# Performance work log

Measured on AMD Instinct MI355X. Metric: run time of the kernel, lower is better.

## Reference

```python
import jax, jax.numpy as jnp
import numpy as np

COUNT = 8  # hardcoded 8x8 patch grid in the original module


def setup_inputs() -> dict:
    key = jax.random.key(0)
    kx, = jax.random.split(key, 1)
    x = jax.random.normal(kx, (8, 64, 512, 512), dtype=jnp.float32)
    gamma = jnp.zeros((1,), dtype=jnp.float32)  # nn.Parameter(torch.zeros(1))
    return {"x": x, "gamma": gamma}


def reference(x, gamma):
    B, C, H, W = x.shape
    s = H // COUNT  # stride; original uses height-derived stride for both dims
    # Extract the 8x8 grid of patches without loops:
    # (B,C,H,W) -> (B,C,cnt,s,cnt,s) -> (B,cnt,cnt,C,s,s) -> (B,P,C,s*s)
    p = x.reshape(B, C, COUNT, s, COUNT, s)
    p = p.transpose(0, 2, 4, 1, 3, 5).reshape(B, COUNT * COUNT, C, s * s)
    # channel-channel energy per patch: [B,P,C,C]
    energy = jnp.einsum('bpci,bpdi->bpcd', p, p)
    # DANet trick: max - energy, then softmax over last dim
    energy_new = jnp.max(energy, axis=-1, keepdims=True) - energy
    attention = jax.nn.softmax(energy_new, axis=-1)
    out = jnp.einsum('bpcd,bpdi->bpci', attention, p)
    # reassemble spatial map
    out = out.reshape(B, COUNT, COUNT, C, s, s)
    out = out.transpose(0, 3, 1, 4, 2, 5).reshape(B, C, H, W)
    # NOTE: in the torch code y = x is an alias and x is overwritten in-place,
    # so the final result is gamma * attended + attended.
    return gamma[0] * out + out
```

## Files before the change

### kernel.cpp

```cpp
#include <hip/hip_runtime.h>


#define NW   512
#define HWs  262144
#define NS   16

typedef __attribute__((ext_vector_type(8)))  __bf16 bf8;
typedef __attribute__((ext_vector_type(4)))  __bf16 bf4;
typedef __attribute__((ext_vector_type(16))) float  f32x16;

#define F4E(v,j) ((j)==0?(v).x:(j)==1?(v).y:(j)==2?(v).z:(v).w)

__device__ __forceinline__ void bar_lgkm() {
  asm volatile("s_waitcnt lgkmcnt(0)" ::: "memory");
  __builtin_amdgcn_s_barrier();
}

extern "C" __global__ __launch_bounds__(512, 4)
void spectralAgg_kernel(const float* __restrict__ x, const float* __restrict__ g,
                        float* __restrict__ out) {
  __shared__ char lds[65536];
  char* sH = lds;
  char* sL = lds + 32768;
  char* sA = lds + 49152;

  const int T   = threadIdx.x;
  const int wv8 = T >> 6;
  const int l   = T & 63;
  const int l31 = l & 31;
  const int hh  = l >> 5;
  const int g2  = (T >> 4) & 3;
  const int e16 = T & 15;

  const int wg = blockIdx.x;
  const int b  = wg >> 6;
  const int pp = wg & 63;
  const size_t pbase = (size_t)b*64*HWs + (size_t)((pp>>3)*64)*NW + (size_t)((pp&7)*64);
  const float* xp = x + pbase;
  float* op = out + pbase;

  float4 ra[8];
#pragma unroll
  for (int k = 0; k < 8; ++k)
    ra[k] = *(const float4*)(xp + (size_t)(k*8+wv8)*HWs + (size_t)g2*NW + e16*4);

  const int q  = wv8 & 3;
  const int kh = wv8 >> 2;
  const int ct = q >> 1, dt = q & 1;
  const char* pA  = sH + (size_t)(ct*32+l31)*512 + kh*256;
  const char* pBh = sH + (size_t)(dt*32+l31)*512 + kh*256;
  const char* pBl = sL + (size_t)(dt*32+l31)*512 + kh*256;
  const int swz1 = (l31 & 15) << 4;

  f32x16 accG, accS;
#pragma unroll
  for (int r = 0; r < 16; ++r) { accG[r] = 0.f; accS[r] = 0.f; }

  for (int st = 0; st < NS; ++st) {
#pragma unroll
    for (int k = 0; k < 8; ++k) {
      const int c = k*8 + wv8;
      const float4 v = ra[k];
      bf4 h, lo;
      h[0]=(__bf16)v.x; h[1]=(__bf16)v.y; h[2]=(__bf16)v.z; h[3]=(__bf16)v.w;
      lo[0]=(__bf16)(v.x-(float)h[0]); lo[1]=(__bf16)(v.y-(float)h[1]);
      lo[2]=(__bf16)(v.z-(float)h[2]); lo[3]=(__bf16)(v.w-(float)h[3]);
      const int off = c*512 + ((g2*128 + e16*8) ^ ((c&15)<<4));
      *(bf4*)(sH+off) = h;
      *(bf4*)(sL+off) = lo;
    }
    const int sn = (st+1 < NS) ? st+1 : st;
#pragma unroll
    for (int k = 0; k < 8; ++k)
      ra[k] = *(const float4*)(xp + (size_t)(k*8+wv8)*HWs + (size_t)(sn*4+g2)*NW + e16*4);
    bar_lgkm();
#pragma unroll
    for (int k0 = 0; k0 < 8; ++k0) {
      const int off = (k0*32 + hh*16) ^ swz1;
      const bf8 a  = *(const bf8*)(pA  + off);
      const bf8 bh = *(const bf8*)(pBh + off);
      const bf8 bl = *(const bf8*)(pBl + off);
      accG = __builtin_amdgcn_mfma_f32_32x32x16_bf16(a, bh, accG, 0, 0, 0);
      accS = __builtin_amdgcn_mfma_f32_32x32x16_bf16(a, bl, accS, 0, 0, 0);
    }
    bar_lgkm();
  }

  float* E_lds = (float*)sH;
  float* S_lds = (float*)sL;
  if (kh == 0) {
#pragma unroll
    for (int r = 0; r < 16; ++r) {
      const int cr = ct*32 + (r&3) + ((r>>2)<<3) + (hh<<2);
      const int d  = dt*32 + l31;
      S_lds[cr*64+d] = accS[r];
      E_lds[cr*64+d] = accG[r] + accS[r];
    }
  }
  bar_lgkm();
  if (kh == 1) {
#pragma unroll
    for (int r = 0; r < 16; ++r) {
      const int cr = ct*32 + (r&3) + ((r>>2)<<3) + (hh<<2);
      const int d  = dt*32 + l31;
      S_lds[cr*64+d] += accS[r];
      E_lds[cr*64+d] += accG[r] + accS[r];
    }
  }
  bar_lgkm();
#pragma unroll
  for (int r = 0; r < 8; ++r) {
    const int c = T >> 3, d = (T&7)*8 + r;
    E_lds[c*64+d] += S_lds[d*64+c];
  }
  bar_lgkm();

  const int quad = (wv8*4+g2) & 15;
  const int rwb  = (wv8*4+g2) >> 4;
#pragma unroll
  for (int k = 0; k < 8; ++k) {
    const int cc = k & 3, mm = k >> 2;
    ra[k] = *(const float4*)(xp + (size_t)(quad*4+cc)*HWs + (size_t)(rwb+mm*2)*NW + e16*4);
  }

  const float gs = 1.0f + g[0];
#pragma unroll 1
  for (int rr = 0; rr < 8; ++rr) {
    const int c = wv8*8 + rr;
    const float e = E_lds[c*64 + l];
    float mn = e;
#pragma unroll
    for (int o = 32; o; o >>= 1) mn = fminf(mn, __shfl_xor(mn, o));
    const float w = __expf(mn - e);
    float s = w;
#pragma unroll
    for (int o = 32; o; o >>= 1) s += __shfl_xor(s, o);
    const float a = gs * w / s;
    *(__bf16*)(sA + c*256 + ((l*2) ^ ((c&15)<<4))) = (__bf16)a;
  }
  bar_lgkm();

  char* sT = sH;
  const char* pP = sT + (size_t)(wv8*32 + l31)*144;

  for (int st = 0; st < NS; ++st) {
#pragma unroll
    for (int mm = 0; mm < 2; ++mm) {
      const int row = rwb + mm*2;
#pragma unroll
      for (int jj = 0; jj < 4; ++jj) {
        const int i = row*64 + e16*4 + jj;
        bf4 qv;
        qv[0] = (__bf16)F4E(ra[mm*4+0], jj);
        qv[1] = (__bf16)F4E(ra[mm*4+1], jj);
        qv[2] = (__bf16)F4E(ra[mm*4+2], jj);
        qv[3] = (__bf16)F4E(ra[mm*4+3], jj);
        *(bf4*)(sT + i*144 + quad*8) = qv;
      }
    }
    const int sn = (st+1 < NS) ? st+1 : st;
#pragma unroll
    for (int k = 0; k < 8; ++k) {
      const int cc = k & 3, mm = k >> 2;
      ra[k] = *(const float4*)(xp + (size_t)(quad*4+cc)*HWs + (size_t)(sn*4+rwb+mm*2)*NW + e16*4);
    }
    bar_lgkm();

    f32x16 oo0, oo1;
#pragma unroll
    for (int r = 0; r < 16; ++r) { oo0[r] = 0.f; oo1[r] = 0.f; }
#pragma unroll
    for (int k0 = 0; k0 < 4; ++k0) {
      const int sAoff = (k0*32 + hh*16) ^ ((l31&15)<<4);
      const bf8 pa = *(const bf8*)(pP + k0*32 + hh*16);
      const bf8 b0 = *(const bf8*)(sA + (size_t)l31*256 + sAoff);
      const bf8 b1 = *(const bf8*)(sA + (size_t)(32+l31)*256 + sAoff);
      oo0 = __builtin_amdgcn_mfma_f32_32x32x16_bf16(pa, b0, oo0, 0, 0, 0);
      oo1 = __builtin_amdgcn_mfma_f32_32x32x16_bf16(pa, b1, oo1, 0, 0, 0);
    }

#pragma unroll
    for (int rq = 0; rq < 4; ++rq) {
      const int iloc = wv8*32 + rq*8 + hh*4;
      const int gi = st*256 + iloc;
      const int grow = gi >> 6, gcol = gi & 63;
      float* oprow = op + (size_t)grow*NW + gcol;
      float4 q0; q0.x = oo0[rq*4+0]; q0.y = oo0[rq*4+1];
                 q0.z = oo0[rq*4+2]; q0.w = oo0[rq*4+3];
      *(float4*)(oprow + (size_t)l31*HWs) = q0;
      float4 q1; q1.x = oo1[rq*4+0]; q1.y = oo1[rq*4+1];
                 q1.z = oo1[rq*4+2]; q1.w = oo1[rq*4+3];
      *(float4*)(oprow + (size_t)(32+l31)*HWs) = q1;
    }
    bar_lgkm();
  }
}

extern "C" void kernel_launch(void* const* d_in, const int* in_sizes, int n_in,
                              void* d_out, int out_size, void* d_ws, size_t ws_size,
                              hipStream_t stream) {
  const float* x = (const float*)d_in[0];
  const float* g = (const float*)d_in[1];
  float* o = (float*)d_out;
  spectralAgg_kernel<<<dim3(512), dim3(512), 0, stream>>>(x, g, o);
}
```

Before: 387.9 us.

## Double-buffer global loads, swizzle transpose LDS, hoist attention fragments, remap blocks

Both phases now keep two register sets of prefetched input tiles, so each global load is issued two stages ahead of use instead of one. The phase-3 transposed patch buffer moves from a padded 144-byte stride to a 256-byte XOR-swizzled layout, intended to avoid LDS bank conflicts. The attention B-fragments are loaded into registers once instead of per stage. Blocks are remapped so consecutive workgroups share a patch column across batch and row, which may change DRAM/L2 locality. Holding two prefetch sets raises register pressure, which could hurt occupancy under the 4-blocks launch bound.

New measurement: 447.5 us. +15.4%, slower.

```diff
diff --git a/kernel.cpp b/kernel.cpp
--- a/kernel.cpp
+++ b/kernel.cpp
@@ -14,6 +14,70 @@
 __device__ __forceinline__ void bar_lgkm() {
   asm volatile("s_waitcnt lgkmcnt(0)" ::: "memory");
   __builtin_amdgcn_s_barrier();
+}
+
+__device__ __forceinline__ void load1(const float* xp, int wv8, int g2, int e16,
+                                      int st, float4 (&R)[8]) {
+#pragma unroll
+  for (int k = 0; k < 8; ++k)
+    R[k] = *(const float4*)(xp + (size_t)(k*8+wv8)*HWs + (size_t)(st*4+g2)*NW + e16*4);
+}
+
+__device__ __forceinline__ void cvt1(char* sH, char* sL, int wv8, int g2, int e16,
+                                     const float4 (&R)[8]) {
+#pragma unroll
+  for (int k = 0; k < 8; ++k) {
+    const int c = k*8 + wv8;
+    const float4 v = R[k];
+    bf4 h, lo;
+    h[0]=(__bf16)v.x; h[1]=(__bf16)v.y; h[2]=(__bf16)v.z; h[3]=(__bf16)v.w;
+    lo[0]=(__bf16)(v.x-(float)h[0]); lo[1]=(__bf16)(v.y-(float)h[1]);
+    lo[2]=(__bf16)(v.z-(float)h[2]); lo[3]=(__bf16)(v.w-(float)h[3]);
+    const int off = c*512 + ((g2*128 + e16*8) ^ ((c&15)<<4));
+    *(bf4*)(sH+off) = h;
+    *(bf4*)(sL+off) = lo;
+  }
+}
+
+__device__ __forceinline__ void mfma1(const char* pA, const char* pBh, const char* pBl,
+                                      int hh, int swz1, f32x16& accG, f32x16& accS) {
+#pragma unroll
+  for (int k0 = 0; k0 < 8; ++k0) {
+    const int off = (k0*32 + hh*16) ^ swz1;
+    const bf8 a  = *(const bf8*)(pA  + off);
+    const bf8 bh = *(const bf8*)(pBh + off);
+    const bf8 bl = *(const bf8*)(pBl + off);
+    accG = __builtin_amdgcn_mfma_f32_32x32x16_bf16(a, bh, accG, 0, 0, 0);
+    accS = __builtin_amdgcn_mfma_f32_32x32x16_bf16(a, bl, accS, 0, 0, 0);
+  }
+}
+
+__device__ __forceinline__ void load3(const float* xp, int quad, int rwb, int e16,
+                                      int st, float4 (&R)[8]) {
+#pragma unroll
+  for (int k = 0; k < 8; ++k) {
+    const int cc = k & 3, mm = k >> 2;
+    R[k] = *(const float4*)(xp + (size_t)(quad*4+cc)*HWs + (size_t)(st*4+rwb+mm*2)*NW + e16*4);
+  }
+}
+
+__device__ __forceinline__ void cvt3(char* sT, int quad, int rwb, int e16,
+                                     const float4 (&R)[8]) {
+#pragma unroll
+  for (int mm = 0; mm < 2; ++mm) {
+    const int row = rwb + mm*2;
+#pragma unroll
+    for (int jj = 0; jj < 4; ++jj) {
+      const int i = row*64 + e16*4 + jj;
+      bf4 qv;
+      qv[0] = (__bf16)F4E(R[mm*4+0], jj);
+      qv[1] = (__bf16)F4E(R[mm*4+1], jj);
+      qv[2] = (__bf16)F4E(R[mm*4+2], jj);
+      qv[3] = (__bf16)F4E(R[mm*4+3], jj);
+      const int sw = ((i & 15) ^ ((i >> 4) & 7)) << 4;
+      *(bf4*)(sT + (i & 127)*256 + ((((i >> 7)*128) + quad*8) ^ sw)) = qv;
+    }
+  }
 }
 
 extern "C" __global__ __launch_bounds__(512, 4)
@@ -32,17 +96,14 @@
   const int g2  = (T >> 4) & 3;
   const int e16 = T & 15;
 
-  const int wg = blockIdx.x;
-  const int b  = wg >> 6;
-  const int pp = wg & 63;
-  const size_t pbase = (size_t)b*64*HWs + (size_t)((pp>>3)*64)*NW + (size_t)((pp&7)*64);
+  const int id = blockIdx.x;
+  const int pc  = id >> 6;
+  const int rem = id & 63;
+  const int b   = rem >> 3;
+  const int pr  = rem & 7;
+  const size_t pbase = (size_t)b*64*HWs + (size_t)(pr*64)*NW + (size_t)(pc*64);
   const float* xp = x + pbase;
   float* op = out + pbase;
-
-  float4 ra[8];
-#pragma unroll
-  for (int k = 0; k < 8; ++k)
-    ra[k] = *(const float4*)(xp + (size_t)(k*8+wv8)*HWs + (size_t)g2*NW + e16*4);
 
   const int q  = wv8 & 3;
   const int kh = wv8 >> 2;
@@ -56,33 +117,21 @@
 #pragma unroll
   for (int r = 0; r < 16; ++r) { accG[r] = 0.f; accS[r] = 0.f; }
 
-  for (int st = 0; st < NS; ++st) {
-#pragma unroll
-    for (int k = 0; k < 8; ++k) {
-      const int c = k*8 + wv8;
-      const float4 v = ra[k];
-      bf4 h, lo;
-      h[0]=(__bf16)v.x; h[1]=(__bf16)v.y; h[2]=(__bf16)v.z; h[3]=(__bf16)v.w;
-      lo[0]=(__bf16)(v.x-(float)h[0]); lo[1]=(__bf16)(v.y-(float)h[1]);
-      lo[2]=(__bf16)(v.z-(float)h[2]); lo[3]=(__bf16)(v.w-(float)h[3]);
-      const int off = c*512 + ((g2*128 + e16*8) ^ ((c&15)<<4));
-      *(bf4*)(sH+off) = h;
-      *(bf4*)(sL+off) = lo;
-    }
-    const int sn = (st+1 < NS) ? st+1 : st;
-#pragma unroll
-    for (int k = 0; k < 8; ++k)
-      ra[k] = *(const float4*)(xp + (size_t)(k*8+wv8)*HWs + (size_t)(sn*4+g2)*NW + e16*4);
-    bar_lgkm();
-#pragma unroll
-    for (int k0 = 0; k0 < 8; ++k0) {
-      const int off = (k0*32 + hh*16) ^ swz1;
-      const bf8 a  = *(const bf8*)(pA  + off);
-      const bf8 bh = *(const bf8*)(pBh + off);
-      const bf8 bl = *(const bf8*)(pBl + off);
-      accG = __builtin_amdgcn_mfma_f32_32x32x16_bf16(a, bh, accG, 0, 0, 0);
-      accS = __builtin_amdgcn_mfma_f32_32x32x16_bf16(a, bl, accS, 0, 0, 0);
-    }
+  float4 rA[8], rB[8];
+  load1(xp, wv8, g2, e16, 0, rA);
+  load1(xp, wv8, g2, e16, 1, rB);
+
+  for (int st = 0; st < NS; st += 2) {
+    cvt1(sH, sL, wv8, g2, e16, rA);
+    if (st + 2 < NS) load1(xp, wv8, g2, e16, st + 2, rA);
+    bar_lgkm();
+    mfma1(pA, pBh, pBl, hh, swz1, accG, accS);
+    bar_lgkm();
+
+    cvt1(sH, sL, wv8, g2, e16, rB);
+    if (st + 3 < NS) load1(xp, wv8, g2, e16, st + 3, rB);
+    bar_lgkm();
+    mfma1(pA, pBh, pBl, hh, swz1, accG, accS);
     bar_lgkm();
   }
 
@@ -117,11 +166,8 @@
 
   const int quad = (wv8*4+g2) & 15;
   const int rwb  = (wv8*4+g2) >> 4;
-#pragma unroll
-  for (int k = 0; k < 8; ++k) {
-    const int cc = k & 3, mm = k >> 2;
-    ra[k] = *(const float4*)(xp + (size_t)(quad*4+cc)*HWs + (size_t)(rwb+mm*2)*NW + e16*4);
-  }
+  load3(xp, quad, rwb, e16, 0, rA);
+  load3(xp, quad, rwb, e16, 1, rB);
 
   const float gs = 1.0f + g[0];
 #pragma unroll 1
@@ -141,56 +187,69 @@
   bar_lgkm();
 
   char* sT = sH;
-  const char* pP = sT + (size_t)(wv8*32 + l31)*144;
-
-  for (int st = 0; st < NS; ++st) {
-#pragma unroll
-    for (int mm = 0; mm < 2; ++mm) {
-      const int row = rwb + mm*2;
-#pragma unroll
-      for (int jj = 0; jj < 4; ++jj) {
-        const int i = row*64 + e16*4 + jj;
-        bf4 qv;
-        qv[0] = (__bf16)F4E(ra[mm*4+0], jj);
-        qv[1] = (__bf16)F4E(ra[mm*4+1], jj);
-        qv[2] = (__bf16)F4E(ra[mm*4+2], jj);
-        qv[3] = (__bf16)F4E(ra[mm*4+3], jj);
-        *(bf4*)(sT + i*144 + quad*8) = qv;
-      }
-    }
-    const int sn = (st+1 < NS) ? st+1 : st;
-#pragma unroll
-    for (int k = 0; k < 8; ++k) {
-      const int cc = k & 3, mm = k >> 2;
-      ra[k] = *(const float4*)(xp + (size_t)(quad*4+cc)*HWs + (size_t)(sn*4+rwb+mm*2)*NW + e16*4);
-    }
-    bar_lgkm();
-
-    f32x16 oo0, oo1;
-#pragma unroll
-    for (int r = 0; r < 16; ++r) { oo0[r] = 0.f; oo1[r] = 0.f; }
-#pragma unroll
-    for (int k0 = 0; k0 < 4; ++k0) {
-      const int sAoff = (k0*32 + hh*16) ^ ((l31&15)<<4);
-      const bf8 pa = *(const bf8*)(pP + k0*32 + hh*16);
-      const bf8 b0 = *(const bf8*)(sA + (size_t)l31*256 + sAoff);
-      const bf8 b1 = *(const bf8*)(sA + (size_t)(32+l31)*256 + sAoff);
-      oo0 = __builtin_amdgcn_mfma_f32_32x32x16_bf16(pa, b0, oo0, 0, 0, 0);
-      oo1 = __builtin_amdgcn_mfma_f32_32x32x16_bf16(pa, b1, oo1, 0, 0, 0);
-    }
-
-#pragma unroll
-    for (int rq = 0; rq < 4; ++rq) {
-      const int iloc = wv8*32 + rq*8 + hh*4;
-      const int gi = st*256 + iloc;
-      const int grow = gi >> 6, gcol = gi & 63;
-      float* oprow = op + (size_t)grow*NW + gcol;
-      float4 q0; q0.x = oo0[rq*4+0]; q0.y = oo0[rq*4+1];
-                 q0.z = oo0[rq*4+2]; q0.w = oo0[rq*4+3];
-      *(float4*)(oprow + (size_t)l31*HWs) = q0;
-      float4 q1; q1.x = oo1[rq*4+0]; q1.y = oo1[rq*4+1];
-                 q1.z = oo1[rq*4+2]; q1.w = oo1[rq*4+3];
-      *(float4*)(oprow + (size_t)(32+l31)*HWs) = q1;
+  const int i3  = wv8*32 + l31;
+  const char* pP = sT + (size_t)(i3 & 127) * 256;
+  const int hb3 = (i3 >> 7) * 128;
+  const int sw3 = ((i3 & 15) ^ ((i3 >> 4) & 7)) << 4;
+
+  bf8 bfr[2][4];
+#pragma unroll
+  for (int c2 = 0; c2 < 2; ++c2)
+#pragma unroll
+    for (int k0 = 0; k0 < 4; ++k0)
+      bfr[c2][k0] = *(const bf8*)(sA + (size_t)(c2*32+l31)*256 +
+                                  ((k0*32 + hh*16) ^ ((l31&15)<<4)));
+
+  for (int st = 0; st < NS; st += 2) {
+    cvt3(sT, quad, rwb, e16, rA);
+    if (st + 2 < NS) load3(xp, quad, rwb, e16, st + 2, rA);
+    bar_lgkm();
+    {
+      f32x16 oo0, oo1;
+#pragma unroll
+      for (int r = 0; r < 16; ++r) { oo0[r] = 0.f; oo1[r] = 0.f; }
+#pragma unroll
+      for (int k0 = 0; k0 < 4; ++k0) {
+        const bf8 pa = *(const bf8*)(pP + ((hb3 + k0*32 + hh*16) ^ sw3));
+        oo0 = __builtin_amdgcn_mfma_f32_32x32x16_bf16(pa, bfr[0][k0], oo0, 0, 0, 0);
+        oo1 = __builtin_amdgcn_mfma_f32_32x32x16_bf16(pa, bfr[1][k0], oo1, 0, 0, 0);
+      }
+#pragma unroll
+      for (int rq = 0; rq < 4; ++rq) {
+        const int iloc = wv8*32 + rq*8 + hh*4;
+        const int gi = st*256 + iloc;
+        float* oprow = op + (size_t)(gi >> 6)*NW + (gi & 63);
+        float4 q0; q0.x=oo0[rq*4+0]; q0.y=oo0[rq*4+1]; q0.z=oo0[rq*4+2]; q0.w=oo0[rq*4+3];
+        *(float4*)(oprow + (size_t)l31*HWs) = q0;
+        float4 q1; q1.x=oo1[rq*4+0]; q1.y=oo1[rq*4+1]; q1.z=oo1[rq*4+2]; q1.w=oo1[rq*4+3];
+        *(float4*)(oprow + (size_t)(32+l31)*HWs) = q1;
+      }
+    }
+    bar_lgkm();
+
+    cvt3(sT, quad, rwb, e16, rB);
+    if (st + 3 < NS) load3(xp, quad, rwb, e16, st + 3, rB);
+    bar_lgkm();
+    {
+      f32x16 oo0, oo1;
+#pragma unroll
+      for (int r = 0; r < 16; ++r) { oo0[r] = 0.f; oo1[r] = 0.f; }
+#pragma unroll
+      for (int k0 = 0; k0 < 4; ++k0) {
+        const bf8 pa = *(const bf8*)(pP + ((hb3 + k0*32 + hh*16) ^ sw3));
+        oo0 = __builtin_amdgcn_mfma_f32_32x32x16_bf16(pa, bfr[0][k0], oo0, 0, 0, 0);
+        oo1 = __builtin_amdgcn_mfma_f32_32x32x16_bf16(pa, bfr[1][k0], oo1, 0, 0, 0);
+      }
+#pragma unroll
+      for (int rq = 0; rq < 4; ++rq) {
+        const int iloc = wv8*32 + rq*8 + hh*4;
+        const int gi = (st+1)*256 + iloc;
+        float* oprow = op + (size_t)(gi >> 6)*NW + (gi & 63);
+        float4 q0; q0.x=oo0[rq*4+0]; q0.y=oo0[rq*4+1]; q0.z=oo0[rq*4+2]; q0.w=oo0[rq*4+3];
+        *(float4*)(oprow + (size_t)l31*HWs) = q0;
+        float4 q1; q1.x=oo1[rq*4+0]; q1.y=oo1[rq*4+1]; q1.z=oo1[rq*4+2]; q1.w=oo1[rq*4+3];
+        *(float4*)(oprow + (size_t)(32+l31)*HWs) = q1;
+      }
     }
     bar_lgkm();
   }
```

## Give each wave private LDS staging to remove per-step block barriers

Applied to the files above, without the earlier changes.

Restructures both GEMM phases so each wave stages its own slice of the patch (spatial chunk) in a private LDS region and computes full 64x64 Gram partials with eight accumulators. The per-step block-wide barriers go away, and the partial Gram matrices are reduced across waves afterwards through serialized LDS accumulation. The second phase keeps the attention operand in registers and transposes per wave. This trades barrier stalls for more registers, 4x more MFMAs per K-step in phase one, a serialized 8-round reduction, and lower occupancy (launch bound 2, 88KB LDS).

New measurement: 420.3 us. 1.08x slower.

```diff
diff --git a/kernel.cpp b/kernel.cpp
--- a/kernel.cpp
+++ b/kernel.cpp
@@ -1,133 +1,137 @@
 #include <hip/hip_runtime.h>
 
 
-#define NW   512
-#define HWs  262144
-#define NS   16
-
+#define NW  512
+#define HWs 262144
+
+typedef __attribute__((ext_vector_type(4)))  __bf16 bf4;
 typedef __attribute__((ext_vector_type(8)))  __bf16 bf8;
-typedef __attribute__((ext_vector_type(4)))  __bf16 bf4;
 typedef __attribute__((ext_vector_type(16))) float  f32x16;
 
-#define F4E(v,j) ((j)==0?(v).x:(j)==1?(v).y:(j)==2?(v).z:(v).w)
-
-__device__ __forceinline__ void bar_lgkm() {
-  asm volatile("s_waitcnt lgkmcnt(0)" ::: "memory");
-  __builtin_amdgcn_s_barrier();
-}
-
-extern "C" __global__ __launch_bounds__(512, 4)
+#define MFMA __builtin_amdgcn_mfma_f32_32x32x16_bf16
+
+extern "C" __global__ __launch_bounds__(512, 2)
 void spectralAgg_kernel(const float* __restrict__ x, const float* __restrict__ g,
                         float* __restrict__ out) {
-  __shared__ char lds[65536];
-  char* sH = lds;
-  char* sL = lds + 32768;
-  char* sA = lds + 49152;
+  __shared__ char lds[90112];
+  char*  sStage = lds;
+  float* E_lds  = (float*)lds;
+  float* S_lds  = (float*)(lds + 16384);
+  char*  sA     = lds + 81920;
 
   const int T   = threadIdx.x;
   const int wv8 = T >> 6;
   const int l   = T & 63;
   const int l31 = l & 31;
   const int hh  = l >> 5;
-  const int g2  = (T >> 4) & 3;
-  const int e16 = T & 15;
+  const int cl  = l >> 3;
+  const int il  = (l & 7) * 4;
 
   const int wg = blockIdx.x;
   const int b  = wg >> 6;
   const int pp = wg & 63;
-  const size_t pbase = (size_t)b*64*HWs + (size_t)((pp>>3)*64)*NW + (size_t)((pp&7)*64);
+  const int pr = pp >> 3, pc = pp & 7;
+  const size_t pbase = (size_t)b * 64 * HWs + (size_t)(pr * 64) * NW + (size_t)(pc * 64);
   const float* xp = x + pbase;
   float* op = out + pbase;
 
-  float4 ra[8];
-#pragma unroll
-  for (int k = 0; k < 8; ++k)
-    ra[k] = *(const float4*)(xp + (size_t)(k*8+wv8)*HWs + (size_t)g2*NW + e16*4);
-
-  const int q  = wv8 & 3;
-  const int kh = wv8 >> 2;
-  const int ct = q >> 1, dt = q & 1;
-  const char* pA  = sH + (size_t)(ct*32+l31)*512 + kh*256;
-  const char* pBh = sH + (size_t)(dt*32+l31)*512 + kh*256;
-  const char* pBl = sL + (size_t)(dt*32+l31)*512 + kh*256;
-  const int swz1 = (l31 & 15) << 4;
-
-  f32x16 accG, accS;
-#pragma unroll
-  for (int r = 0; r < 16; ++r) { accG[r] = 0.f; accS[r] = 0.f; }
-
-  for (int st = 0; st < NS; ++st) {
-#pragma unroll
-    for (int k = 0; k < 8; ++k) {
-      const int c = k*8 + wv8;
-      const float4 v = ra[k];
+  char* myStage = sStage + wv8 * 10240;
+  char* myHi = myStage;
+  char* myLo = myStage + 5120;
+
+#define LOADST(stv, R)                                                          \
+  {                                                                             \
+    const int r_ = wv8 * 8 + ((stv) >> 1);                                      \
+    const int ch_ = ((stv) & 1) * 32;                                           \
+    const float* base_ = xp + (size_t)r_ * NW + ch_ + il;                       \
+    _Pragma("unroll")                                                           \
+    for (int j = 0; j < 8; ++j)                                                 \
+      R[j] = *(const float4*)(base_ + (size_t)(cl + 8 * j) * HWs);              \
+  }
+
+  f32x16 G00, G01, G10, G11, S00, S01, S10, S11;
+#pragma unroll
+  for (int i = 0; i < 16; ++i) {
+    G00[i]=0.f; G01[i]=0.f; G10[i]=0.f; G11[i]=0.f;
+    S00[i]=0.f; S01[i]=0.f; S10[i]=0.f; S11[i]=0.f;
+  }
+
+  float4 rA[8], rB[8];
+  LOADST(0, rA);
+
+  for (int st = 0; st < 16; ++st) {
+    if (st + 1 < 16) LOADST(st + 1, rB);
+#pragma unroll
+    for (int j = 0; j < 8; ++j) {
+      const int c = cl + 8 * j;
+      const float4 v = rA[j];
       bf4 h, lo;
       h[0]=(__bf16)v.x; h[1]=(__bf16)v.y; h[2]=(__bf16)v.z; h[3]=(__bf16)v.w;
       lo[0]=(__bf16)(v.x-(float)h[0]); lo[1]=(__bf16)(v.y-(float)h[1]);
       lo[2]=(__bf16)(v.z-(float)h[2]); lo[3]=(__bf16)(v.w-(float)h[3]);
-      const int off = c*512 + ((g2*128 + e16*8) ^ ((c&15)<<4));
-      *(bf4*)(sH+off) = h;
-      *(bf4*)(sL+off) = lo;
-    }
-    const int sn = (st+1 < NS) ? st+1 : st;
-#pragma unroll
-    for (int k = 0; k < 8; ++k)
-      ra[k] = *(const float4*)(xp + (size_t)(k*8+wv8)*HWs + (size_t)(sn*4+g2)*NW + e16*4);
-    bar_lgkm();
-#pragma unroll
-    for (int k0 = 0; k0 < 8; ++k0) {
-      const int off = (k0*32 + hh*16) ^ swz1;
-      const bf8 a  = *(const bf8*)(pA  + off);
-      const bf8 bh = *(const bf8*)(pBh + off);
-      const bf8 bl = *(const bf8*)(pBl + off);
-      accG = __builtin_amdgcn_mfma_f32_32x32x16_bf16(a, bh, accG, 0, 0, 0);
-      accS = __builtin_amdgcn_mfma_f32_32x32x16_bf16(a, bl, accS, 0, 0, 0);
-    }
-    bar_lgkm();
-  }
-
-  float* E_lds = (float*)sH;
-  float* S_lds = (float*)sL;
-  if (kh == 0) {
-#pragma unroll
-    for (int r = 0; r < 16; ++r) {
-      const int cr = ct*32 + (r&3) + ((r>>2)<<3) + (hh<<2);
-      const int d  = dt*32 + l31;
-      S_lds[cr*64+d] = accS[r];
-      E_lds[cr*64+d] = accG[r] + accS[r];
-    }
-  }
-  bar_lgkm();
-  if (kh == 1) {
-#pragma unroll
-    for (int r = 0; r < 16; ++r) {
-      const int cr = ct*32 + (r&3) + ((r>>2)<<3) + (hh<<2);
-      const int d  = dt*32 + l31;
-      S_lds[cr*64+d] += accS[r];
-      E_lds[cr*64+d] += accG[r] + accS[r];
-    }
-  }
-  bar_lgkm();
-#pragma unroll
-  for (int r = 0; r < 8; ++r) {
-    const int c = T >> 3, d = (T&7)*8 + r;
-    E_lds[c*64+d] += S_lds[d*64+c];
-  }
-  bar_lgkm();
-
-  const int quad = (wv8*4+g2) & 15;
-  const int rwb  = (wv8*4+g2) >> 4;
-#pragma unroll
-  for (int k = 0; k < 8; ++k) {
-    const int cc = k & 3, mm = k >> 2;
-    ra[k] = *(const float4*)(xp + (size_t)(quad*4+cc)*HWs + (size_t)(rwb+mm*2)*NW + e16*4);
-  }
+      *(bf4*)(myHi + c * 80 + il * 2) = h;
+      *(bf4*)(myLo + c * 80 + il * 2) = lo;
+    }
+#pragma unroll
+    for (int kk = 0; kk < 2; ++kk) {
+      const int ko = kk * 32 + hh * 16;
+      const bf8 a0 = *(const bf8*)(myHi + (size_t)l31 * 80 + ko);
+      const bf8 a1 = *(const bf8*)(myHi + (size_t)(32 + l31) * 80 + ko);
+      const bf8 q0 = *(const bf8*)(myLo + (size_t)l31 * 80 + ko);
+      const bf8 q1 = *(const bf8*)(myLo + (size_t)(32 + l31) * 80 + ko);
+      G00 = MFMA(a0, a0, G00, 0, 0, 0);
+      G01 = MFMA(a0, a1, G01, 0, 0, 0);
+      G10 = MFMA(a1, a0, G10, 0, 0, 0);
+      G11 = MFMA(a1, a1, G11, 0, 0, 0);
+      S00 = MFMA(a0, q0, S00, 0, 0, 0);
+      S01 = MFMA(a0, q1, S01, 0, 0, 0);
+      S10 = MFMA(a1, q0, S10, 0, 0, 0);
+      S11 = MFMA(a1, q1, S11, 0, 0, 0);
+    }
+#pragma unroll
+    for (int e = 0; e < 8; ++e) rA[e] = rB[e];
+  }
+
+  __syncthreads();
+  {
+    float4 z; z.x=0.f; z.y=0.f; z.z=0.f; z.w=0.f;
+    float4* pz = (float4*)lds;
+#pragma unroll
+    for (int k = 0; k < 4; ++k) pz[T * 4 + k] = z;
+  }
+  __syncthreads();
+  for (int rd = 0; rd < 8; ++rd) {
+    if (wv8 == rd) {
+#pragma unroll
+      for (int i = 0; i < 16; ++i) {
+        const int rr = (i & 3) + ((i >> 2) << 3) + (hh << 2);
+        E_lds[rr * 64 + l31]             += G00[i] + S00[i];
+        E_lds[rr * 64 + 32 + l31]        += G01[i] + S01[i];
+        E_lds[(32 + rr) * 64 + l31]      += G10[i] + S10[i];
+        E_lds[(32 + rr) * 64 + 32 + l31] += G11[i] + S11[i];
+        S_lds[rr * 64 + l31]             += S00[i];
+        S_lds[rr * 64 + 32 + l31]        += S01[i];
+        S_lds[(32 + rr) * 64 + l31]      += S10[i];
+        S_lds[(32 + rr) * 64 + 32 + l31] += S11[i];
+      }
+    }
+    __syncthreads();
+  }
+  {
+    const int c = T >> 3;
+#pragma unroll
+    for (int k = 0; k < 8; ++k) {
+      const int d = (T & 7) * 8 + k;
+      E_lds[c * 64 + d] += S_lds[d * 64 + c];
+    }
+  }
+  __syncthreads();
 
   const float gs = 1.0f + g[0];
 #pragma unroll 1
-  for (int rr = 0; rr < 8; ++rr) {
-    const int c = wv8*8 + rr;
-    const float e = E_lds[c*64 + l];
+  for (int rr2 = 0; rr2 < 8; ++rr2) {
+    const int c = wv8 * 8 + rr2;
+    const float e = E_lds[c * 64 + l];
     float mn = e;
 #pragma unroll
     for (int o = 32; o; o >>= 1) mn = fminf(mn, __shfl_xor(mn, o));
@@ -136,63 +140,54 @@
 #pragma unroll
     for (int o = 32; o; o >>= 1) s += __shfl_xor(s, o);
     const float a = gs * w / s;
-    *(__bf16*)(sA + c*256 + ((l*2) ^ ((c&15)<<4))) = (__bf16)a;
-  }
-  bar_lgkm();
-
-  char* sT = sH;
-  const char* pP = sT + (size_t)(wv8*32 + l31)*144;
-
-  for (int st = 0; st < NS; ++st) {
-#pragma unroll
-    for (int mm = 0; mm < 2; ++mm) {
-      const int row = rwb + mm*2;
-#pragma unroll
-      for (int jj = 0; jj < 4; ++jj) {
-        const int i = row*64 + e16*4 + jj;
-        bf4 qv;
-        qv[0] = (__bf16)F4E(ra[mm*4+0], jj);
-        qv[1] = (__bf16)F4E(ra[mm*4+1], jj);
-        qv[2] = (__bf16)F4E(ra[mm*4+2], jj);
-        qv[3] = (__bf16)F4E(ra[mm*4+3], jj);
-        *(bf4*)(sT + i*144 + quad*8) = qv;
+    *(__bf16*)(sA + c * 128 + ((l * 2) ^ ((c & 7) << 4))) = (__bf16)a;
+  }
+  __syncthreads();
+
+  bf8 bfr[2][4];
+#pragma unroll
+  for (int c2 = 0; c2 < 2; ++c2)
+#pragma unroll
+    for (int k0 = 0; k0 < 4; ++k0)
+      bfr[c2][k0] = *(const bf8*)(sA + (size_t)(c2 * 32 + l31) * 128 +
+                                  ((k0 * 32 + hh * 16) ^ ((l31 & 7) << 4)));
+
+  LOADST(0, rA);
+  for (int st = 0; st < 16; ++st) {
+    if (st + 1 < 16) LOADST(st + 1, rB);
+#pragma unroll
+    for (int j = 0; j < 8; ++j) {
+      const int c = cl + 8 * j;
+      const float4 v = rA[j];
+      *(__bf16*)(myStage + (size_t)(il + 0) * 144 + c * 2) = (__bf16)v.x;
+      *(__bf16*)(myStage + (size_t)(il + 1) * 144 + c * 2) = (__bf16)v.y;
+      *(__bf16*)(myStage + (size_t)(il + 2) * 144 + c * 2) = (__bf16)v.z;
+      *(__bf16*)(myStage + (size_t)(il + 3) * 144 + c * 2) = (__bf16)v.w;
+    }
+    f32x16 o0, o1;
+#pragma unroll
+    for (int i = 0; i < 16; ++i) { o0[i] = 0.f; o1[i] = 0.f; }
+#pragma unroll
+    for (int ks = 0; ks < 4; ++ks) {
+      const bf8 pa = *(const bf8*)(myStage + (size_t)l31 * 144 + ks * 32 + hh * 16);
+      o0 = MFMA(pa, bfr[0][ks], o0, 0, 0, 0);
+      o1 = MFMA(pa, bfr[1][ks], o1, 0, 0, 0);
+    }
+    {
+      const int r  = wv8 * 8 + (st >> 1);
+      const int ch = (st & 1) * 32;
+#pragma unroll
+      for (int rq = 0; rq < 4; ++rq) {
+        const int io = rq * 8 + hh * 4;
+        float* orow = op + (size_t)r * NW + ch + io;
+        float4 q0; q0.x=o0[rq*4+0]; q0.y=o0[rq*4+1]; q0.z=o0[rq*4+2]; q0.w=o0[rq*4+3];
+        *(float4*)(orow + (size_t)l31 * HWs) = q0;
+        float4 q1; q1.x=o1[rq*4+0]; q1.y=o1[rq*4+1]; q1.z=o1[rq*4+2]; q1.w=o1[rq*4+3];
+        *(float4*)(orow + (size_t)(32 + l31) * HWs) = q1;
       }
     }
-    const int sn = (st+1 < NS) ? st+1 : st;
-#pragma unroll
-    for (int k = 0; k < 8; ++k) {
-      const int cc = k & 3, mm = k >> 2;
-      ra[k] = *(const float4*)(xp + (size_t)(quad*4+cc)*HWs + (size_t)(sn*4+rwb+mm*2)*NW + e16*4);
-    }
-    bar_lgkm();
-
-    f32x16 oo0, oo1;
-#pragma unroll
-    for (int r = 0; r < 16; ++r) { oo0[r] = 0.f; oo1[r] = 0.f; }
-#pragma unroll
-    for (int k0 = 0; k0 < 4; ++k0) {
-      const int sAoff = (k0*32 + hh*16) ^ ((l31&15)<<4);
-      const bf8 pa = *(const bf8*)(pP + k0*32 + hh*16);
-      const bf8 b0 = *(const bf8*)(sA + (size_t)l31*256 + sAoff);
-      const bf8 b1 = *(const bf8*)(sA + (size_t)(32+l31)*256 + sAoff);
-      oo0 = __builtin_amdgcn_mfma_f32_32x32x16_bf16(pa, b0, oo0, 0, 0, 0);
-      oo1 = __builtin_amdgcn_mfma_f32_32x32x16_bf16(pa, b1, oo1, 0, 0, 0);
-    }
-
-#pragma unroll
-    for (int rq = 0; rq < 4; ++rq) {
-      const int iloc = wv8*32 + rq*8 + hh*4;
-      const int gi = st*256 + iloc;
-      const int grow = gi >> 6, gcol = gi & 63;
-      float* oprow = op + (size_t)grow*NW + gcol;
-      float4 q0; q0.x = oo0[rq*4+0]; q0.y = oo0[rq*4+1];
-                 q0.z = oo0[rq*4+2]; q0.w = oo0[rq*4+3];
-      *(float4*)(oprow + (size_t)l31*HWs) = q0;
-      float4 q1; q1.x = oo1[rq*4+0]; q1.y = oo1[rq*4+1];
-                 q1.z = oo1[rq*4+2]; q1.w = oo1[rq*4+3];
-      *(float4*)(oprow + (size_t)(32+l31)*HWs) = q1;
-    }
-    bar_lgkm();
+#pragma unroll
+    for (int e = 0; e < 8; ++e) rA[e] = rB[e];
   }
 }
 
```
